# Optimization experiments

Measured on AMD Instinct MI355X. Metric: run time of the kernel, lower is better.

The kernel has to match this reference:

```python
import jax, jax.numpy as jnp
import numpy as np

N = 100000   # nodes
E = 1000000  # edges (before self-loops)
D_IN = 16
H, C = 2, 64  # heads, hidden per head
EPS = 1e-5    # BatchNorm eps
SLOPE = 0.2   # LeakyReLU negative slope (GATConv default)


def setup_inputs() -> dict:
    key = jax.random.key(0)
    ks = jax.random.split(key, 40)
    rn = lambda k, s, sc=0.1: jax.random.normal(k, s, jnp.float32) * sc
    inp = {}
    inp["x"] = jax.random.normal(ks[0], (N, D_IN), jnp.float32)
    inp["edge_index"] = jax.random.randint(ks[1], (2, E), 0, N)
    i = 2
    for l, din in ((1, D_IN), (2, C), (3, C)):
        inp[f"W{l}"] = rn(ks[i], (din, H * C)); i += 1
        inp[f"as{l}"] = rn(ks[i], (H, C)); i += 1
        inp[f"ad{l}"] = rn(ks[i], (H, C)); i += 1
        inp[f"b{l}"] = jnp.zeros((C,), jnp.float32)
        inp[f"g{l}"] = jnp.ones((C,), jnp.float32)   # BN gamma
        inp[f"be{l}"] = jnp.zeros((C,), jnp.float32) # BN beta
    inp["mW1"] = rn(ks[i], (C + 5, C)); i += 1
    inp["mb1"] = jnp.zeros((C,), jnp.float32)
    inp["mW2"] = rn(ks[i], (C, C)); i += 1
    inp["mb2"] = jnp.zeros((C,), jnp.float32)
    inp["pW"] = rn(ks[i], (C, 1)); i += 1
    inp["pb"] = jnp.zeros((1,), jnp.float32)
    inp["vW"] = rn(ks[i], (C, 1)); i += 1
    inp["vb"] = jnp.zeros((1,), jnp.float32)
    return inp


def gat(x, src, dst, W, att_s, att_d, bias):
    # GATConv, heads=H, concat=False (mean over heads). Messages flow src->dst.
    h = (x @ W).reshape(-1, H, C)               # [N,H,C]
    a_s = jnp.sum(h * att_s, -1)                # [N,H]
    a_d = jnp.sum(h * att_d, -1)                # [N,H]
    e = jax.nn.leaky_relu(a_s[src] + a_d[dst], SLOPE)  # [Etot,H]
    e = e - jax.ops.segment_max(e, dst, num_segments=N)[dst]
    ee = jnp.exp(e)
    alpha = ee / (jax.ops.segment_sum(ee, dst, num_segments=N)[dst] + 1e-16)
    msg = h[src] * alpha[:, :, None]            # [Etot,H,C]
    out = jax.ops.segment_sum(msg, dst, num_segments=N)  # [N,H,C]
    return out.mean(1) + bias                   # [N,C]


def bn(h, g, b):
    m = h.mean(0)
    v = jnp.mean((h - m) ** 2, 0)  # biased variance (torch BN normalization)
    return (h - m) * jax.lax.rsqrt(v + EPS) * g + b


def reference(x, edge_index, W1, as1, ad1, b1, g1, be1,
              W2, as2, ad2, b2, g2, be2, W3, as3, ad3, b3, g3, be3,
              mW1, mb1, mW2, mb2, pW, pb, vW, vb):
    loops = jnp.arange(N)
    src = jnp.concatenate([edge_index[0], loops])  # add_self_loops=True
    dst = jnp.concatenate([edge_index[1], loops])
    ctx = x[:, 9:14]  # context features [N,5]
    h = jax.nn.relu(bn(gat(x, src, dst, W1, as1, ad1, b1), g1, be1))
    h = jax.nn.relu(bn(gat(h, src, dst, W2, as2, ad2, b2), g2, be2))
    h = jax.nn.relu(bn(gat(h, src, dst, W3, as3, ad3, b3), g3, be3))
    # dropout is identity in eval reference
    h = jnp.concatenate([h, ctx], axis=1)          # [N, C+5]
    h = jax.nn.relu(h @ mW1 + mb1) @ mW2 + mb2     # MLP
    logits = (h @ pW + pb).squeeze(-1)             # [N]
    value = (h @ vW + vb).squeeze(-1)              # [N]
    return logits, value
```

## Files before the change

### kernel.cpp

```cpp
#include <hip/hip_runtime.h>
#include <hip/hip_fp16.h>


__device__ __forceinline__ float leaky(float x) { return x > 0.f ? x : 0.2f * x; }

typedef float f32x4 __attribute__((ext_vector_type(4)));
typedef _Float16 f16x8 __attribute__((ext_vector_type(8)));

#define BCAP 4096
#define NSL 256

__global__ void bucket_hist(const int* __restrict__ dst, int* __restrict__ bcnt, int E) {
  __shared__ int cnt[512];
  int t = threadIdx.x;
  cnt[t] = 0; cnt[t + 256] = 0;
  __syncthreads();
  for (int e = blockIdx.x * blockDim.x + t; e < E; e += gridDim.x * blockDim.x)
    atomicAdd(&cnt[dst[e] >> 8], 1);
  __syncthreads();
  for (int i = t; i < 512; i += 256)
    if (cnt[i]) atomicAdd(&bcnt[i], cnt[i]);
}

__global__ void bucket_scan(const int* __restrict__ bcnt, int* __restrict__ boff,
                            int* __restrict__ bcur, int nbk) {
  __shared__ int temp[512];
  int t = threadIdx.x;
  int v = (t < nbk) ? bcnt[t] : 0;
  temp[t] = v;
  __syncthreads();
  for (int off = 1; off < 512; off <<= 1) {
    int add = (t >= off) ? temp[t - off] : 0;
    __syncthreads();
    temp[t] += add;
    __syncthreads();
  }
  if (t < nbk) {
    int ex = temp[t] - v;
    boff[t] = ex;
    bcur[t] = ex;
  }
}

__global__ __launch_bounds__(256) void bin_scatter(
    const int* __restrict__ src, const int* __restrict__ dst,
    int* __restrict__ bcur, int2* __restrict__ ebuf, int E) {
  __shared__ int cnt[512];
  __shared__ int base[512];
  int t = threadIdx.x;
  int beg = blockIdx.x * 8192;
  int end = min(E, beg + 8192);
  cnt[t] = 0; cnt[t + 256] = 0;
  __syncthreads();
  for (int e = beg + t; e < end; e += 256)
    atomicAdd(&cnt[dst[e] >> 8], 1);
  __syncthreads();
  for (int i = t; i < 512; i += 256) {
    base[i] = cnt[i] ? atomicAdd(&bcur[i], cnt[i]) : 0;
    cnt[i] = 0;
  }
  __syncthreads();
  for (int e = beg + t; e < end; e += 256) {
    int d = dst[e];
    int bk = d >> 8;
    int off = atomicAdd(&cnt[bk], 1);
    ebuf[base[bk] + off] = make_int2(src[e], d);
  }
}

__global__ __launch_bounds__(256) void bucket_sort(
    const int2* __restrict__ ebuf, const int* __restrict__ boff,
    int* __restrict__ col, int* __restrict__ row_ptr, int E, int n, int nbk) {
  __shared__ int2 eds[BCAP];
  __shared__ int dcnt[256];
  __shared__ int dbase[256];
  __shared__ int dexcl[256];
  int b = blockIdx.x, t = threadIdx.x;
  int S = boff[b];
  int Eend = (b + 1 < nbk) ? boff[b + 1] : E;
  int cnt = min(Eend - S, BCAP);
  for (int i = t; i < cnt; i += 256) eds[i] = ebuf[S + i];
  dcnt[t] = 0;
  __syncthreads();
  for (int i = t; i < cnt; i += 256) atomicAdd(&dcnt[eds[i].y & 255], 1);
  __syncthreads();
  int v = dcnt[t];
  dbase[t] = v;
  __syncthreads();
  for (int off = 1; off < 256; off <<= 1) {
    int add = (t >= off) ? dbase[t - off] : 0;
    __syncthreads();
    dbase[t] += add;
    __syncthreads();
  }
  int excl = dbase[t] - v;
  int d = (b << 8) + t;
  if (d < n) row_ptr[d] = S + excl;
  if (b == nbk - 1 && t == 0) row_ptr[n] = E;
  dcnt[t] = 0;
  dexcl[t] = excl;
  __syncthreads();
  for (int i = t; i < cnt; i += 256) {
    int2 e = eds[i];
    int dl = e.y & 255;
    int off = atomicAdd(&dcnt[dl], 1);
    col[S + dexcl[dl] + off] = e.x;
  }
}

__global__ __launch_bounds__(256) void bn_stats(const float* __restrict__ h,
                                                float* __restrict__ stats, int n) {
  __shared__ float ssum[64], ssq[64];
  int t = threadIdx.x;
  if (t < 64) { ssum[t] = 0.f; ssq[t] = 0.f; }
  __syncthreads();
  const float4* h4 = (const float4*)h;
  size_t total4 = (size_t)n * 16;
  size_t stride = (size_t)gridDim.x * blockDim.x;
  int cbase = ((int)(((size_t)blockIdx.x * blockDim.x + t) & 15)) * 4;
  float s0 = 0.f, s1 = 0.f, s2 = 0.f, s3 = 0.f;
  float q0 = 0.f, q1 = 0.f, q2 = 0.f, q3 = 0.f;
  for (size_t i = (size_t)blockIdx.x * blockDim.x + t; i < total4; i += stride) {
    float4 v = h4[i];
    s0 += v.x; q0 = fmaf(v.x, v.x, q0);
    s1 += v.y; q1 = fmaf(v.y, v.y, q1);
    s2 += v.z; q2 = fmaf(v.z, v.z, q2);
    s3 += v.w; q3 = fmaf(v.w, v.w, q3);
  }
  atomicAdd(&ssum[cbase + 0], s0); atomicAdd(&ssq[cbase + 0], q0);
  atomicAdd(&ssum[cbase + 1], s1); atomicAdd(&ssq[cbase + 1], q1);
  atomicAdd(&ssum[cbase + 2], s2); atomicAdd(&ssq[cbase + 2], q2);
  atomicAdd(&ssum[cbase + 3], s3); atomicAdd(&ssq[cbase + 3], q3);
  __syncthreads();
  if (t < 64) {
    stats[blockIdx.x * 128 + t] = ssum[t];
    stats[blockIdx.x * 128 + 64 + t] = ssq[t];
  }
}

__global__ void bn_finalize(const float* __restrict__ stats, const float* __restrict__ g,
                            const float* __restrict__ be, float* __restrict__ scsh,
                            float inv_n) {
  __shared__ float red[128];
  int t = threadIdx.x;
  int c = t & 63;
  int off = (t >> 6) * 64;
  float acc = 0.f;
  for (int b = 0; b < NSL; b++) acc += stats[b * 128 + off + c];
  red[t] = acc;
  __syncthreads();
  if (t < 64) {
    float mean = red[t] * inv_n;
    float var = red[64 + t] * inv_n - mean * mean;
    float sc = rsqrtf(var + 1e-5f) * g[t];
    scsh[t] = sc;
    scsh[64 + t] = be[t] - mean * sc;
  }
}

template <int K, bool BN>
__global__ __launch_bounds__(256) void gat_project_mfma(
    const float* __restrict__ act, const float* __restrict__ scsh,
    const float* __restrict__ W,
    const float* __restrict__ att_s, const float* __restrict__ att_d,
    __half2* __restrict__ hb, float* __restrict__ as_,
    float* __restrict__ ad_, int n) {
  constexpr int KE = (K < 32) ? 32 : K;
  constexpr int KP = KE + 8;
  constexpr int STAGE = 64 * KP * 2 + 128 * KP * 2;
  constexpr int HSZ = 64 * 136 * 2;
  constexpr int LDSZ = (STAGE > HSZ) ? STAGE : HSZ;
  __shared__ __align__(16) char ldsb[LDSZ];
  __shared__ float attS[256];
  __half* aH = (__half*)ldsb;
  __half* wT = (__half*)(ldsb + 64 * KP * 2);
  __half* hS = (__half*)ldsb;

  int t = threadIdx.x;
  int node0 = blockIdx.x * 64;
  int rows = min(64, n - node0);

  constexpr int ACH = 64 * KE / 4;
  for (int i = t; i < ACH; i += 256) {
    int r = i / (KE / 4), kc = i % (KE / 4);
    float4 v = make_float4(0.f, 0.f, 0.f, 0.f);
    if (r < rows && kc * 4 < K)
      v = *(const float4*)&act[(size_t)(node0 + r) * K + kc * 4];
    if (BN) {
      float4 sc4 = *(const float4*)&scsh[kc * 4];
      float4 sh4 = *(const float4*)&scsh[64 + kc * 4];
      v.x = fmaxf(fmaf(v.x, sc4.x, sh4.x), 0.f);
      v.y = fmaxf(fmaf(v.y, sc4.y, sh4.y), 0.f);
      v.z = fmaxf(fmaf(v.z, sc4.z, sh4.z), 0.f);
      v.w = fmaxf(fmaf(v.w, sc4.w, sh4.w), 0.f);
    }
    __half2 h01 = __floats2half2_rn(v.x, v.y);
    __half2 h23 = __floats2half2_rn(v.z, v.w);
    uint2 pk = make_uint2(__builtin_bit_cast(unsigned, h01),
                          __builtin_bit_cast(unsigned, h23));
    *(uint2*)&aH[r * KP + kc * 4] = pk;
  }
  for (int i = t; i < KE * 128; i += 256) {
    int k = i >> 7, c = i & 127;
    float wv = (k < K) ? W[k * 128 + c] : 0.f;
    wT[c * KP + k] = __float2half(wv);
  }
  attS[t] = (t < 128) ? att_s[t] : att_d[t - 128];
  __syncthreads();

  int w = t >> 6, l = t & 63;
  int cl = l & 15, r4 = l >> 4;
  int w16 = w * 16;

  f32x4 acc[8] = {};
#pragma unroll
  for (int ks = 0; ks < KE / 32; ks++) {
    f16x8 av = *(const f16x8*)&aH[(w16 + cl) * KP + ks * 32 + r4 * 8];
#pragma unroll
    for (int ct = 0; ct < 8; ct++) {
      f16x8 bv = *(const f16x8*)&wT[(ct * 16 + cl) * KP + ks * 32 + r4 * 8];
      acc[ct] = __builtin_amdgcn_mfma_f32_16x16x32_f16(av, bv, acc[ct], 0, 0, 0);
    }
  }

  float ats[8], atd[8];
#pragma unroll
  for (int ct = 0; ct < 8; ct++) {
    ats[ct] = attS[ct * 16 + cl];
    atd[ct] = attS[128 + ct * 16 + cl];
  }
#pragma unroll
  for (int i = 0; i < 4; i++) {
    float s0 = 0.f, s1 = 0.f, d0 = 0.f, d1 = 0.f;
#pragma unroll
    for (int ct = 0; ct < 4; ct++) {
      s0 = fmaf(acc[ct][i], ats[ct], s0);
      d0 = fmaf(acc[ct][i], atd[ct], d0);
      s1 = fmaf(acc[ct + 4][i], ats[ct + 4], s1);
      d1 = fmaf(acc[ct + 4][i], atd[ct + 4], d1);
    }
#pragma unroll
    for (int off = 1; off < 16; off <<= 1) {
      s0 += __shfl_xor(s0, off); s1 += __shfl_xor(s1, off);
      d0 += __shfl_xor(d0, off); d1 += __shfl_xor(d1, off);
    }
    int rloc = w16 + r4 * 4 + i;
    if (rloc < rows) {
      int row = node0 + rloc;
      if (cl == 0) as_[row * 2] = s0;
      else if (cl == 1) as_[row * 2 + 1] = s1;
      else if (cl == 2) ad_[row * 2] = d0;
      else if (cl == 3) ad_[row * 2 + 1] = d1;
    }
  }

  __syncthreads();
#pragma unroll
  for (int ct = 0; ct < 8; ct++)
#pragma unroll
    for (int i = 0; i < 4; i++)
      hS[(w16 + r4 * 4 + i) * 136 + ct * 16 + cl] = __float2half(acc[ct][i]);
  __syncthreads();
#pragma unroll
  for (int it = 0; it < 4; it++) {
    int flat = t + it * 256;
    int nd = flat >> 4, ch = flat & 15;
    if (nd < rows)
      *(uint4*)((char*)hb + (((size_t)(node0 + nd)) << 8) + (ch << 4)) =
          *(const uint4*)((const char*)hS + nd * 272 + (ch << 4));
  }
}

__device__ __forceinline__ void fma8(float* a, float my, uint4 raw) {
  float2 f;
  f = __half22float2(__builtin_bit_cast(__half2, raw.x)); a[0] = fmaf(my, f.x, a[0]); a[1] = fmaf(my, f.y, a[1]);
  f = __half22float2(__builtin_bit_cast(__half2, raw.y)); a[2] = fmaf(my, f.x, a[2]); a[3] = fmaf(my, f.y, a[3]);
  f = __half22float2(__builtin_bit_cast(__half2, raw.z)); a[4] = fmaf(my, f.x, a[4]); a[5] = fmaf(my, f.y, a[5]);
  f = __half22float2(__builtin_bit_cast(__half2, raw.w)); a[6] = fmaf(my, f.x, a[6]); a[7] = fmaf(my, f.y, a[7]);
}

__global__ __launch_bounds__(256) void gat_aggregate(
    const __half2* __restrict__ hb,
    const float* __restrict__ as_, const float* __restrict__ ad_,
    const int* __restrict__ row_ptr, const int* __restrict__ col,
    const float* __restrict__ bias, float* __restrict__ out, int n) {
  int w = (int)((blockIdx.x * blockDim.x + threadIdx.x) >> 6);
  int lane = threadIdx.x & 63;
  int g = lane >> 4, q = lane & 15;
  int d = w * 4 + g;
  if (d >= n) return;
  int hidx = (q >= 8) ? 1 : 0;
  int beg = row_ptr[d], end = row_ptr[d + 1];
  const uint4* hb4 = (const uint4*)hb;

  float ad_my = ad_[d * 2 + hidx];

  float a[8] = {};
  float asv = as_[d * 2 + hidx];
  float my = __expf(leaky(asv + ad_my));
  uint4 raw = hb4[(size_t)d * 16 + q];
  fma8(a, my, raw);
  float dpart = my;

  int k = beg;
  for (; k + 3 < end; k += 4) {
    int s0 = col[k], s1 = col[k + 1], s2 = col[k + 2], s3 = col[k + 3];
    float e0 = as_[s0 * 2 + hidx];
    float e1 = as_[s1 * 2 + hidx];
    float e2 = as_[s2 * 2 + hidx];
    float e3 = as_[s3 * 2 + hidx];
    uint4 r0 = hb4[(size_t)s0 * 16 + q];
    uint4 r1 = hb4[(size_t)s1 * 16 + q];
    uint4 r2 = hb4[(size_t)s2 * 16 + q];
    uint4 r3 = hb4[(size_t)s3 * 16 + q];
    float m0 = __expf(leaky(e0 + ad_my));
    float m1 = __expf(leaky(e1 + ad_my));
    float m2 = __expf(leaky(e2 + ad_my));
    float m3 = __expf(leaky(e3 + ad_my));
    fma8(a, m0, r0); fma8(a, m1, r1); fma8(a, m2, r2); fma8(a, m3, r3);
    dpart += m0 + m1 + m2 + m3;
  }
  for (; k < end; k++) {
    int s = col[k];
    float e = as_[s * 2 + hidx];
    uint4 r = hb4[(size_t)s * 16 + q];
    float m = __expf(leaky(e + ad_my));
    fma8(a, m, r);
    dpart += m;
  }

  float b[8];
#pragma unroll
  for (int i = 0; i < 8; i++) b[i] = __shfl_xor(a[i], 8);
  float denO = __shfl_xor(dpart, 8);

  if (q < 8) {
    float rr0 = 1.f / (dpart + 1e-16f), rr1 = 1.f / (denO + 1e-16f);
    float4 bl = *(const float4*)&bias[q * 8];
    float4 bh = *(const float4*)&bias[q * 8 + 4];
    f32x4 o0, o1;
    o0.x = 0.5f * (a[0] * rr0 + b[0] * rr1) + bl.x;
    o0.y = 0.5f * (a[1] * rr0 + b[1] * rr1) + bl.y;
    o0.z = 0.5f * (a[2] * rr0 + b[2] * rr1) + bl.z;
    o0.w = 0.5f * (a[3] * rr0 + b[3] * rr1) + bl.w;
    o1.x = 0.5f * (a[4] * rr0 + b[4] * rr1) + bh.x;
    o1.y = 0.5f * (a[5] * rr0 + b[5] * rr1) + bh.y;
    o1.z = 0.5f * (a[6] * rr0 + b[6] * rr1) + bh.z;
    o1.w = 0.5f * (a[7] * rr0 + b[7] * rr1) + bh.w;
    f32x4* outp = (f32x4*)&out[(size_t)d * 64 + q * 8];
    __builtin_nontemporal_store(o0, outp);
    __builtin_nontemporal_store(o1, outp + 1);
  }
}

__global__ __launch_bounds__(256) void mlp_head_tiled(
    const float* __restrict__ h3raw, const float* __restrict__ scsh,
    const float* __restrict__ x,
    const float* __restrict__ mW1, const float* __restrict__ mb1,
    const float* __restrict__ mW2, const float* __restrict__ mb2,
    const float* __restrict__ pW, const float* __restrict__ pb,
    const float* __restrict__ vW, const float* __restrict__ vb,
    float* __restrict__ out, int n) {
  __shared__ float lds[13632];
  float* a1  = lds;
  float* ctx = lds + 4352;
  float* a2  = lds + 4864;
  float* w1  = lds + 9216;
  float* w2  = lds;

  int t = threadIdx.x;
  int node0 = blockIdx.x * 64;
  int rows = min(64, n - node0);

#pragma unroll
  for (int i = 0; i < 4; i++) {
    int flat = t + i * 256;
    int r = flat >> 4, kc = flat & 15;
    float4 v = make_float4(0.f, 0.f, 0.f, 0.f);
    if (r < rows) v = *(const float4*)&h3raw[(size_t)(node0 + r) * 64 + kc * 4];
    float4 sc4 = *(const float4*)&scsh[kc * 4];
    float4 sh4 = *(const float4*)&scsh[64 + kc * 4];
    v.x = fmaxf(fmaf(v.x, sc4.x, sh4.x), 0.f);
    v.y = fmaxf(fmaf(v.y, sc4.y, sh4.y), 0.f);
    v.z = fmaxf(fmaf(v.z, sc4.z, sh4.z), 0.f);
    v.w = fmaxf(fmaf(v.w, sc4.w, sh4.w), 0.f);
    *(float4*)&a1[r * 68 + kc * 4] = v;
  }
  for (int i = t; i < 320; i += 256) {
    int r = i / 5, j = i % 5;
    ctx[r * 8 + j] = (r < rows) ? x[(size_t)(node0 + r) * 16 + 9 + j] : 0.f;
  }
#pragma unroll
  for (int i = 0; i < 5; i++) {
    int flat = t + i * 256;
    if (flat < 1104) *(float4*)&w1[flat * 4] = *(const float4*)&mW1[flat * 4];
  }
  __syncthreads();

  int tc = t & 15, tr = t >> 4;
  int c0 = tc * 4, r0 = tr * 4;

  float acc[4][4] = {};
  for (int k = 0; k < 64; k += 4) {
    float4 av[4], wv[4];
#pragma unroll
    for (int i = 0; i < 4; i++) av[i] = *(const float4*)&a1[(r0 + i) * 68 + k];
#pragma unroll
    for (int j = 0; j < 4; j++) wv[j] = *(const float4*)&w1[(k + j) * 64 + c0];
#pragma unroll
    for (int i = 0; i < 4; i++) {
      const float* ai = (const float*)&av[i];
#pragma unroll
      for (int kk = 0; kk < 4; kk++) {
        const float* wr = (const float*)&wv[kk];
        acc[i][0] = fmaf(ai[kk], wr[0], acc[i][0]);
        acc[i][1] = fmaf(ai[kk], wr[1], acc[i][1]);
        acc[i][2] = fmaf(ai[kk], wr[2], acc[i][2]);
        acc[i][3] = fmaf(ai[kk], wr[3], acc[i][3]);
      }
    }
  }
#pragma unroll
  for (int k = 64; k < 69; k++) {
    float4 wv = *(const float4*)&w1[k * 64 + c0];
    const float* wr = (const float*)&wv;
#pragma unroll
    for (int i = 0; i < 4; i++) {
      float a = ctx[(r0 + i) * 8 + (k - 64)];
      acc[i][0] = fmaf(a, wr[0], acc[i][0]);
      acc[i][1] = fmaf(a, wr[1], acc[i][1]);
      acc[i][2] = fmaf(a, wr[2], acc[i][2]);
      acc[i][3] = fmaf(a, wr[3], acc[i][3]);
    }
  }
  float b1v0 = mb1[c0], b1v1 = mb1[c0 + 1], b1v2 = mb1[c0 + 2], b1v3 = mb1[c0 + 3];
#pragma unroll
  for (int i = 0; i < 4; i++) {
    float4 t1;
    t1.x = fmaxf(acc[i][0] + b1v0, 0.f);
    t1.y = fmaxf(acc[i][1] + b1v1, 0.f);
    t1.z = fmaxf(acc[i][2] + b1v2, 0.f);
    t1.w = fmaxf(acc[i][3] + b1v3, 0.f);
    *(float4*)&a2[(r0 + i) * 68 + c0] = t1;
  }
  __syncthreads();

#pragma unroll
  for (int i = 0; i < 4; i++) {
    int flat = t + i * 256;
    *(float4*)&w2[flat * 4] = *(const float4*)&mW2[flat * 4];
  }
  __syncthreads();

  float acc2[4][4] = {};
  for (int k = 0; k < 64; k += 4) {
    float4 av[4], wv[4];
#pragma unroll
    for (int i = 0; i < 4; i++) av[i] = *(const float4*)&a2[(r0 + i) * 68 + k];
#pragma unroll
    for (int j = 0; j < 4; j++) wv[j] = *(const float4*)&w2[(k + j) * 64 + c0];
#pragma unroll
    for (int i = 0; i < 4; i++) {
      const float* ai = (const float*)&av[i];
#pragma unroll
      for (int kk = 0; kk < 4; kk++) {
        const float* wr = (const float*)&wv[kk];
        acc2[i][0] = fmaf(ai[kk], wr[0], acc2[i][0]);
        acc2[i][1] = fmaf(ai[kk], wr[1], acc2[i][1]);
        acc2[i][2] = fmaf(ai[kk], wr[2], acc2[i][2]);
        acc2[i][3] = fmaf(ai[kk], wr[3], acc2[i][3]);
      }
    }
  }

  float b2v[4], pwv[4], vwv[4];
#pragma unroll
  for (int j = 0; j < 4; j++) {
    b2v[j] = mb2[c0 + j];
    pwv[j] = pW[c0 + j];
    vwv[j] = vW[c0 + j];
  }
  float p[4], v[4];
#pragma unroll
  for (int i = 0; i < 4; i++) {
    float ps = 0.f, vs = 0.f;
#pragma unroll
    for (int j = 0; j < 4; j++) {
      float u = acc2[i][j] + b2v[j];
      ps = fmaf(u, pwv[j], ps);
      vs = fmaf(u, vwv[j], vs);
    }
    p[i] = ps; v[i] = vs;
  }
#pragma unroll
  for (int off = 1; off < 16; off <<= 1) {
#pragma unroll
    for (int i = 0; i < 4; i++) {
      p[i] += __shfl_xor(p[i], off);
      v[i] += __shfl_xor(v[i], off);
    }
  }
  if (tc == 0) {
    float pbs = pb[0], vbs = vb[0];
#pragma unroll
    for (int i = 0; i < 4; i++) {
      int r = r0 + i;
      if (r < rows) {
        out[node0 + r] = p[i] + pbs;
        out[n + node0 + r] = v[i] + vbs;
      }
    }
  }
}

extern "C" void kernel_launch(void* const* d_in, const int* in_sizes, int n_in,
                              void* d_out, int out_size, void* d_ws, size_t ws_size,
                              hipStream_t stream) {
  const float* x = (const float*)d_in[0];
  const int* ei = (const int*)d_in[1];
  const float* W[3]  = {(const float*)d_in[2],  (const float*)d_in[8],  (const float*)d_in[14]};
  const float* AS[3] = {(const float*)d_in[3],  (const float*)d_in[9],  (const float*)d_in[15]};
  const float* AD[3] = {(const float*)d_in[4],  (const float*)d_in[10], (const float*)d_in[16]};
  const float* B[3]  = {(const float*)d_in[5],  (const float*)d_in[11], (const float*)d_in[17]};
  const float* G[3]  = {(const float*)d_in[6],  (const float*)d_in[12], (const float*)d_in[18]};
  const float* BE[3] = {(const float*)d_in[7],  (const float*)d_in[13], (const float*)d_in[19]};
  const float* mW1 = (const float*)d_in[20];
  const float* mb1 = (const float*)d_in[21];
  const float* mW2 = (const float*)d_in[22];
  const float* mb2 = (const float*)d_in[23];
  const float* pW  = (const float*)d_in[24];
  const float* pb  = (const float*)d_in[25];
  const float* vW  = (const float*)d_in[26];
  const float* vb  = (const float*)d_in[27];

  const int N = in_sizes[0] / 16;
  const int E = in_sizes[1] / 2;
  const int* srcp = ei;
  const int* dstp = ei + E;

  float* bufB  = (float*)d_ws;
  float* hbuf  = bufB + (size_t)N * 64;
  float* as_   = hbuf + (size_t)N * 64;
  float* ad_   = as_ + (size_t)N * 2;
  float* stats = ad_ + (size_t)N * 2;
  float* scsh  = stats + NSL * 128;
  int* row_ptr = (int*)(scsh + 128);
  int* bcnt    = row_ptr + (N + 1);
  int* boff    = bcnt + 512;
  int* bcur    = boff + 512;
  int* col     = bcur + 512;
  int2* ebuf   = (int2*)(col + E);
  __half2* hb  = (__half2*)hbuf;

  const int nbk = (N + 255) >> 8;
  const float inv_n = 1.0f / (float)N;

  hipMemsetAsync(bcnt, 0, sizeof(int) * 512, stream);
  bucket_hist<<<256, 256, 0, stream>>>(dstp, bcnt, E);
  bucket_scan<<<1, 512, 0, stream>>>(bcnt, boff, bcur, nbk);
  bin_scatter<<<(E + 8191) / 8192, 256, 0, stream>>>(srcp, dstp, bcur, ebuf, E);
  bucket_sort<<<nbk, 256, 0, stream>>>(ebuf, boff, col, row_ptr, E, N, nbk);

  const int tiles = (N + 63) / 64;
  const int agg_blocks = (N + 15) / 16;

  for (int l = 0; l < 3; l++) {
    if (l == 0)
      gat_project_mfma<16, false><<<tiles, 256, 0, stream>>>(x, scsh, W[l], AS[l], AD[l],
                                                             hb, as_, ad_, N);
    else
      gat_project_mfma<64, true><<<tiles, 256, 0, stream>>>(bufB, scsh, W[l], AS[l], AD[l],
                                                            hb, as_, ad_, N);
    gat_aggregate<<<agg_blocks, 256, 0, stream>>>(hb, as_, ad_, row_ptr, col,
                                                  B[l], bufB, N);
    bn_stats<<<NSL, 256, 0, stream>>>(bufB, stats, N);
    bn_finalize<<<1, 128, 0, stream>>>(stats, G[l], BE[l], scsh, inv_n);
  }

  mlp_head_tiled<<<tiles, 256, 0, stream>>>(bufB, scsh, x, mW1, mb1, mW2, mb2,
                                            pW, pb, vW, vb, (float*)d_out, N);
}
```

Baseline: 471.5 us.

## Degree-sort nodes within buckets for aggregation balance and fuse BN finalize into stats

Bucket sort now builds a per-bucket permutation that groups destination nodes by in-degree (capped bins). The aggregate kernel visits nodes through this permutation, so the four 16-lane groups in a wave handle nodes with similar degree and divergence across the wave's edge loop shrinks. Separately, the BN finalize kernel is merged into bn_stats using a last-block-done atomic counter, which removes one launch per layer. The costs are an extra indirection per node, less locality when writing output rows, and a grid-wide counter that must be reset correctly between layers.

Result: slower. 618.6 us (+31.2%).

```diff
diff --git a/kernel.cpp b/kernel.cpp
--- a/kernel.cpp
+++ b/kernel.cpp
@@ -70,17 +70,21 @@
 
 __global__ __launch_bounds__(256) void bucket_sort(
     const int2* __restrict__ ebuf, const int* __restrict__ boff,
-    int* __restrict__ col, int* __restrict__ row_ptr, int E, int n, int nbk) {
+    int* __restrict__ col, int* __restrict__ row_ptr, int* __restrict__ perm,
+    int E, int n, int nbk) {
   __shared__ int2 eds[BCAP];
   __shared__ int dcnt[256];
   __shared__ int dbase[256];
   __shared__ int dexcl[256];
+  __shared__ int dgh[32];
   int b = blockIdx.x, t = threadIdx.x;
   int S = boff[b];
   int Eend = (b + 1 < nbk) ? boff[b + 1] : E;
   int cnt = min(Eend - S, BCAP);
   for (int i = t; i < cnt; i += 256) eds[i] = ebuf[S + i];
   dcnt[t] = 0;
+  if (t < 32) dgh[t] = 0;
+  perm[(b << 8) + t] = n;
   __syncthreads();
   for (int i = t; i < cnt; i += 256) atomicAdd(&dcnt[eds[i].y & 255], 1);
   __syncthreads();
@@ -95,8 +99,19 @@
   }
   int excl = dbase[t] - v;
   int d = (b << 8) + t;
-  if (d < n) row_ptr[d] = S + excl;
+  bool valid = (d < n);
+  if (valid) row_ptr[d] = S + excl;
   if (b == nbk - 1 && t == 0) row_ptr[n] = E;
+  int bin = min(v, 31);
+  int within = 0;
+  if (valid) within = atomicAdd(&dgh[bin], 1);
+  __syncthreads();
+  if (t == 0) {
+    int s = 0;
+    for (int i = 0; i < 32; i++) { int c = dgh[i]; dgh[i] = s; s += c; }
+  }
+  __syncthreads();
+  if (valid) perm[(b << 8) + dgh[bin] + within] = d;
   dcnt[t] = 0;
   dexcl[t] = excl;
   __syncthreads();
@@ -108,9 +123,13 @@
   }
 }
 
-__global__ __launch_bounds__(256) void bn_stats(const float* __restrict__ h,
-                                                float* __restrict__ stats, int n) {
+__global__ __launch_bounds__(256) void bn_stats(
+    const float* __restrict__ h, float* __restrict__ stats,
+    const float* __restrict__ g, const float* __restrict__ be,
+    float* __restrict__ scsh, int* __restrict__ ctr, float inv_n, int n) {
   __shared__ float ssum[64], ssq[64];
+  __shared__ float red2[256];
+  __shared__ int lastf;
   int t = threadIdx.x;
   if (t < 64) { ssum[t] = 0.f; ssq[t] = 0.f; }
   __syncthreads();
@@ -136,22 +155,27 @@
     stats[blockIdx.x * 128 + t] = ssum[t];
     stats[blockIdx.x * 128 + 64 + t] = ssq[t];
   }
-}
-
-__global__ void bn_finalize(const float* __restrict__ stats, const float* __restrict__ g,
-                            const float* __restrict__ be, float* __restrict__ scsh,
-                            float inv_n) {
-  __shared__ float red[128];
-  int t = threadIdx.x;
-  int c = t & 63;
-  int off = (t >> 6) * 64;
+  __threadfence();
+  __syncthreads();
+  if (t == 0) {
+    int old = atomicAdd(ctr, 1);
+    lastf = (old == NSL - 1) ? 1 : 0;
+  }
+  __syncthreads();
+  if (!lastf) return;
+  if (t == 0) *ctr = 0;
+  __threadfence();
+  int c = t & 127, half = t >> 7;
   float acc = 0.f;
-  for (int b = 0; b < NSL; b++) acc += stats[b * 128 + off + c];
-  red[t] = acc;
+  for (int bsl = half * 128; bsl < half * 128 + 128; bsl++)
+    acc += stats[bsl * 128 + c];
+  red2[t] = acc;
   __syncthreads();
   if (t < 64) {
-    float mean = red[t] * inv_n;
-    float var = red[64 + t] * inv_n - mean * mean;
+    float s  = red2[t] + red2[t + 128];
+    float sq = red2[64 + t] + red2[64 + t + 128];
+    float mean = s * inv_n;
+    float var = sq * inv_n - mean * mean;
     float sc = rsqrtf(var + 1e-5f) * g[t];
     scsh[t] = sc;
     scsh[64 + t] = be[t] - mean * sc;
@@ -283,11 +307,14 @@
     const __half2* __restrict__ hb,
     const float* __restrict__ as_, const float* __restrict__ ad_,
     const int* __restrict__ row_ptr, const int* __restrict__ col,
-    const float* __restrict__ bias, float* __restrict__ out, int n) {
-  int w = (int)((blockIdx.x * blockDim.x + threadIdx.x) >> 6);
+    const int* __restrict__ perm,
+    const float* __restrict__ bias, float* __restrict__ out, int n, int npad) {
+  int wv = (int)((blockIdx.x * blockDim.x + threadIdx.x) >> 6);
   int lane = threadIdx.x & 63;
   int g = lane >> 4, q = lane & 15;
-  int d = w * 4 + g;
+  int idx = wv * 4 + g;
+  if (idx >= npad) return;
+  int d = perm[idx];
   if (d >= n) return;
   int hidx = (q >= 8) ? 1 : 0;
   int beg = row_ptr[d], end = row_ptr[d + 1];
@@ -538,6 +565,9 @@
   const int* srcp = ei;
   const int* dstp = ei + E;
 
+  const int nbk = (N + 255) >> 8;
+  const int npad = nbk << 8;
+
   float* bufB  = (float*)d_ws;
   float* hbuf  = bufB + (size_t)N * 64;
   float* as_   = hbuf + (size_t)N * 64;
@@ -546,23 +576,24 @@
   float* scsh  = stats + NSL * 128;
   int* row_ptr = (int*)(scsh + 128);
   int* bcnt    = row_ptr + (N + 1);
-  int* boff    = bcnt + 512;
+  int* ctr     = bcnt + 512;
+  int* boff    = ctr + 4;
   int* bcur    = boff + 512;
-  int* col     = bcur + 512;
+  int* perm    = bcur + 512;
+  int* col     = perm + npad;
   int2* ebuf   = (int2*)(col + E);
   __half2* hb  = (__half2*)hbuf;
 
-  const int nbk = (N + 255) >> 8;
   const float inv_n = 1.0f / (float)N;
 
-  hipMemsetAsync(bcnt, 0, sizeof(int) * 512, stream);
+  hipMemsetAsync(bcnt, 0, sizeof(int) * 516, stream);
   bucket_hist<<<256, 256, 0, stream>>>(dstp, bcnt, E);
   bucket_scan<<<1, 512, 0, stream>>>(bcnt, boff, bcur, nbk);
   bin_scatter<<<(E + 8191) / 8192, 256, 0, stream>>>(srcp, dstp, bcur, ebuf, E);
-  bucket_sort<<<nbk, 256, 0, stream>>>(ebuf, boff, col, row_ptr, E, N, nbk);
+  bucket_sort<<<nbk, 256, 0, stream>>>(ebuf, boff, col, row_ptr, perm, E, N, nbk);
 
   const int tiles = (N + 63) / 64;
-  const int agg_blocks = (N + 15) / 16;
+  const int agg_blocks = npad / 16;
 
   for (int l = 0; l < 3; l++) {
     if (l == 0)
@@ -571,10 +602,9 @@
     else
       gat_project_mfma<64, true><<<tiles, 256, 0, stream>>>(bufB, scsh, W[l], AS[l], AD[l],
                                                             hb, as_, ad_, N);
-    gat_aggregate<<<agg_blocks, 256, 0, stream>>>(hb, as_, ad_, row_ptr, col,
-                                                  B[l], bufB, N);
-    bn_stats<<<NSL, 256, 0, stream>>>(bufB, stats, N);
-    bn_finalize<<<1, 128, 0, stream>>>(stats, G[l], BE[l], scsh, inv_n);
+    gat_aggregate<<<agg_blocks, 256, 0, stream>>>(hb, as_, ad_, row_ptr, col, perm,
+                                                  B[l], bufB, N, npad);
+    bn_stats<<<NSL, 256, 0, stream>>>(bufB, stats, G[l], BE[l], scsh, ctr, inv_n, N);
   }
 
   mlp_head_tiled<<<tiles, 256, 0, stream>>>(bufB, scsh, x, mW1, mb1, mW2, mb2,
```
